# Performance work log

Measured on AMD Instinct MI355X. Metric: run time of the kernel, lower is better.

## Reference

```python
import jax, jax.numpy as jnp
import numpy as np

B, C, U, N = 8, 64, 3, 512


def setup_inputs() -> dict:
    key = jax.random.key(0)
    k1, k2, k3, k4 = jax.random.split(key, 4)
    x = jax.random.normal(k1, (B, C, U, N), dtype=jnp.float32)
    # nn.Linear weights [out, in], applied as x @ W.T over channel dim
    s = 1.0 / np.sqrt(C)
    Wq = jax.random.uniform(k2, (C, C), dtype=jnp.float32, minval=-s, maxval=s)
    Wk = jax.random.uniform(k3, (C, C), dtype=jnp.float32, minval=-s, maxval=s)
    Wv = jax.random.uniform(k4, (C, C), dtype=jnp.float32, minval=-s, maxval=s)
    return {"x": x, "Wq": Wq, "Wk": Wk, "Wv": Wv}


def reference(x, Wq, Wk, Wv):
    # VNLinear: Linear over channel dim (dim 1), no bias: out[b,d,u,n] = sum_c x[b,c,u,n] W[d,c]
    def vn_linear(t, W):
        return jnp.einsum('bcun,dc->bdun', t, W)

    q = vn_linear(x, Wq)
    k = vn_linear(x, Wk)
    v = vn_linear(x, Wv)
    scale = x.shape[1] ** (-0.5)  # in_channels^-0.5
    # contraction over tiny vector-neuron dim u=3
    attn_logits = jnp.einsum('bcui,bcuj->bcij', q, k) * scale  # [B,C,N,N]
    attn_weights = jax.nn.softmax(attn_logits, axis=-1)
    out = jnp.einsum('bcij,bcuj->bcui', attn_weights, v)  # [B,C,U,N]
    return x + out
```

## Files before the change

kernel.cpp:

```cpp
#include <hip/hip_runtime.h>

#define BB 8
#define CC 64
#define UU 3
#define NN 512
#define POS (UU * NN)
#define QKV_ELEMS (BB * CC * POS)
#define SCALE2 0.1803368801111793f

typedef float f2 __attribute__((ext_vector_type(2)));

__global__ __launch_bounds__(256) void proj_kernel(
    const float* __restrict__ x,
    const float* __restrict__ Wq,
    const float* __restrict__ Wk,
    const float* __restrict__ Wv,
    float* __restrict__ ws)
{
    const int blk  = blockIdx.x;
    const int b    = blk & 7;
    const int rest = blk >> 3;
    const int d0   = (rest / 6) * 4;
    const int chunk= rest % 6;
    const int p    = chunk * 256 + threadIdx.x;

    const float* wq = Wq + (size_t)d0 * CC;
    const float* wk = Wk + (size_t)d0 * CC;
    const float* wv = Wv + (size_t)d0 * CC;
    const float* xb = x + (size_t)b * CC * POS + p;

    float qa[4] = {0.f, 0.f, 0.f, 0.f};
    float ka[4] = {0.f, 0.f, 0.f, 0.f};
    float va[4] = {0.f, 0.f, 0.f, 0.f};

    #pragma unroll 4
    for (int c = 0; c < CC; ++c) {
        float xv = xb[c * POS];
        #pragma unroll
        for (int r = 0; r < 4; ++r) {
            qa[r] = fmaf(xv, wq[r * CC + c], qa[r]);
            ka[r] = fmaf(xv, wk[r * CC + c], ka[r]);
            va[r] = fmaf(xv, wv[r * CC + c], va[r]);
        }
    }

    float* qs = ws;
    float* ks = ws + QKV_ELEMS;
    float* vs = ws + 2 * QKV_ELEMS;
    #pragma unroll
    for (int r = 0; r < 4; ++r) {
        size_t base = (size_t)(b * CC + d0 + r) * POS + p;
        qs[base] = qa[r] * SCALE2;
        ks[base] = ka[r];
        vs[base] = va[r];
    }
}

__global__ __launch_bounds__(256) void attn_kernel(
    const float* __restrict__ x,
    const float* __restrict__ ws,
    float* __restrict__ out)
{
    const int bd  = blockIdx.x;
    const int tid = threadIdx.x;

    __shared__ __align__(16) float ks[UU][NN];
    __shared__ __align__(16) float vs[UU][NN];
    __shared__ float4 part[NN];

    const float* qsg = ws + (size_t)bd * POS;
    const float* ksg = ws + QKV_ELEMS     + (size_t)bd * POS;
    const float* vsg = ws + 2 * QKV_ELEMS + (size_t)bd * POS;

    {
        const float4* kg4 = (const float4*)ksg;
        const float4* vg4 = (const float4*)vsg;
        float4* ks4 = (float4*)&ks[0][0];
        float4* vs4 = (float4*)&vs[0][0];
        #pragma unroll
        for (int it = 0; it < 3; ++it) {
            int idx = tid + it * 256;
            if (idx < 384) ks4[idx] = kg4[idx];
            else           vs4[idx - 384] = vg4[idx - 384];
        }
    }
    __syncthreads();

    const int h    = tid & 3;
    const int slot = tid >> 2;

    f2 Q0[8], Q1[8], Q2[8];
    #pragma unroll
    for (int m = 0; m < 8; ++m) {
        int i = slot + m * 64;
        float a = qsg[i], b = qsg[NN + i], c = qsg[2 * NN + i];
        Q0[m] = (f2){a, a};
        Q1[m] = (f2){b, b};
        Q2[m] = (f2){c, c};
    }

    f2 L[8], A0[8], A1[8], A2[8];
    #pragma unroll
    for (int m = 0; m < 8; ++m) {
        L[m] = (f2){0.f, 0.f};  A0[m] = (f2){0.f, 0.f};
        A1[m] = (f2){0.f, 0.f}; A2[m] = (f2){0.f, 0.f};
    }

    const float4* k0p = (const float4*)&ks[0][0] + h * 32;
    const float4* k1p = (const float4*)&ks[1][0] + h * 32;
    const float4* k2p = (const float4*)&ks[2][0] + h * 32;
    const float4* v0p = (const float4*)&vs[0][0] + h * 32;
    const float4* v1p = (const float4*)&vs[1][0] + h * 32;
    const float4* v2p = (const float4*)&vs[2][0] + h * 32;
    const int t0 = 2 * h;

    for (int tt = 0; tt < 32; ++tt) {
        const int t = (tt + t0) & 31;
        float4 k0 = k0p[t];
        float4 k1 = k1p[t];
        float4 k2 = k2p[t];
        float4 v0 = v0p[t];
        float4 v1 = v1p[t];
        float4 v2 = v2p[t];

        f2 k0a = (f2){k0.x, k0.y}, k0b = (f2){k0.z, k0.w};
        f2 k1a = (f2){k1.x, k1.y}, k1b = (f2){k1.z, k1.w};
        f2 k2a = (f2){k2.x, k2.y}, k2b = (f2){k2.z, k2.w};
        f2 v0a = (f2){v0.x, v0.y}, v0b = (f2){v0.z, v0.w};
        f2 v1a = (f2){v1.x, v1.y}, v1b = (f2){v1.z, v1.w};
        f2 v2a = (f2){v2.x, v2.y}, v2b = (f2){v2.z, v2.w};

        #pragma unroll
        for (int m = 0; m < 8; ++m) {
            f2 sa = __builtin_elementwise_fma(Q0[m], k0a,
                     __builtin_elementwise_fma(Q1[m], k1a, Q2[m] * k2a));
            f2 sb = __builtin_elementwise_fma(Q0[m], k0b,
                     __builtin_elementwise_fma(Q1[m], k1b, Q2[m] * k2b));

            f2 pa = (f2){__builtin_amdgcn_exp2f(sa.x), __builtin_amdgcn_exp2f(sa.y)};
            f2 pb = (f2){__builtin_amdgcn_exp2f(sb.x), __builtin_amdgcn_exp2f(sb.y)};

            L[m]  = L[m] + pa + pb;
            A0[m] = __builtin_elementwise_fma(pa, v0a,
                      __builtin_elementwise_fma(pb, v0b, A0[m]));
            A1[m] = __builtin_elementwise_fma(pa, v1a,
                      __builtin_elementwise_fma(pb, v1b, A1[m]));
            A2[m] = __builtin_elementwise_fma(pa, v2a,
                      __builtin_elementwise_fma(pb, v2b, A2[m]));
        }
    }

    #pragma unroll
    for (int m = 0; m < 8; ++m) {
        float l  = L[m].x  + L[m].y;
        float a0 = A0[m].x + A0[m].y;
        float a1 = A1[m].x + A1[m].y;
        float a2 = A2[m].x + A2[m].y;

        l  += __shfl_xor(l,  1);  l  += __shfl_xor(l,  2);
        a0 += __shfl_xor(a0, 1);  a0 += __shfl_xor(a0, 2);
        a1 += __shfl_xor(a1, 1);  a1 += __shfl_xor(a1, 2);
        a2 += __shfl_xor(a2, 1);  a2 += __shfl_xor(a2, 2);

        if (h == 0) part[slot + m * 64] = make_float4(a0, a1, a2, l);
    }
    __syncthreads();

    const float* xd = x   + (size_t)bd * POS;
    float*       od = out + (size_t)bd * POS;
    #pragma unroll
    for (int w = 0; w < 2; ++w) {
        int i = tid + w * 256;
        float4 P = part[i];
        float inv = 1.0f / P.w;
        od[i]          = xd[i]          + P.x * inv;
        od[NN + i]     = xd[NN + i]     + P.y * inv;
        od[2 * NN + i] = xd[2 * NN + i] + P.z * inv;
    }
}

__global__ __launch_bounds__(256) void vn_attn_fused(
    const float* __restrict__ x,
    const float* __restrict__ Wq,
    const float* __restrict__ Wk,
    const float* __restrict__ Wv,
    float* __restrict__ out)
{
    const int bd  = blockIdx.x;
    const int b   = bd / CC;
    const int d   = bd % CC;
    const int tid = threadIdx.x;

    __shared__ float wq[CC], wk[CC], wv[CC];
    __shared__ float qs[UU][NN];
    __shared__ float ks[UU][NN];
    __shared__ float vs[UU][NN];

    if (tid < CC) {
        wq[tid] = Wq[d * CC + tid];
        wk[tid] = Wk[d * CC + tid];
        wv[tid] = Wv[d * CC + tid];
    }
    __syncthreads();

    const float* xb = x + (size_t)b * CC * POS;
    for (int p = tid; p < POS; p += 256) {
        float qa = 0.f, ka = 0.f, va = 0.f;
        #pragma unroll 8
        for (int c = 0; c < CC; ++c) {
            float xv = xb[c * POS + p];
            qa = fmaf(xv, wq[c], qa);
            ka = fmaf(xv, wk[c], ka);
            va = fmaf(xv, wv[c], va);
        }
        int u = p >> 9, n = p & (NN - 1);
        qs[u][n] = qa * SCALE2;
        ks[u][n] = ka;
        vs[u][n] = va;
    }
    __syncthreads();

    for (int i = tid; i < NN; i += 256) {
        float q0 = qs[0][i], q1 = qs[1][i], q2 = qs[2][i];
        float l = 0.f, a0 = 0.f, a1 = 0.f, a2 = 0.f;
        for (int j = 0; j < NN; j += 4) {
            float4 k0 = *(const float4*)&ks[0][j];
            float4 k1 = *(const float4*)&ks[1][j];
            float4 k2 = *(const float4*)&ks[2][j];
            float4 v0 = *(const float4*)&vs[0][j];
            float4 v1 = *(const float4*)&vs[1][j];
            float4 v2 = *(const float4*)&vs[2][j];
            float s0 = fmaf(q0, k0.x, fmaf(q1, k1.x, q2 * k2.x));
            float s1 = fmaf(q0, k0.y, fmaf(q1, k1.y, q2 * k2.y));
            float s2 = fmaf(q0, k0.z, fmaf(q1, k1.z, q2 * k2.z));
            float s3 = fmaf(q0, k0.w, fmaf(q1, k1.w, q2 * k2.w));
            float p0 = __builtin_amdgcn_exp2f(s0);
            float p1 = __builtin_amdgcn_exp2f(s1);
            float p2 = __builtin_amdgcn_exp2f(s2);
            float p3 = __builtin_amdgcn_exp2f(s3);
            l += p0 + p1 + p2 + p3;
            a0 = fmaf(p0, v0.x, fmaf(p1, v0.y, fmaf(p2, v0.z, fmaf(p3, v0.w, a0))));
            a1 = fmaf(p0, v1.x, fmaf(p1, v1.y, fmaf(p2, v1.z, fmaf(p3, v1.w, a1))));
            a2 = fmaf(p0, v2.x, fmaf(p1, v2.y, fmaf(p2, v2.z, fmaf(p3, v2.w, a2))));
        }
        float inv = 1.0f / l;
        size_t obase = ((size_t)(b * CC + d) * UU) * NN + i;
        const float* xd = xb + (size_t)d * POS;
        out[obase]          = xd[i]          + a0 * inv;
        out[obase + NN]     = xd[NN + i]     + a1 * inv;
        out[obase + 2 * NN] = xd[2 * NN + i] + a2 * inv;
    }
}

extern "C" void kernel_launch(void* const* d_in, const int* in_sizes, int n_in,
                              void* d_out, int out_size, void* d_ws, size_t ws_size,
                              hipStream_t stream) {
    const float* x  = (const float*)d_in[0];
    const float* Wq = (const float*)d_in[1];
    const float* Wk = (const float*)d_in[2];
    const float* Wv = (const float*)d_in[3];
    float* out = (float*)d_out;

    if (ws_size >= (size_t)3 * QKV_ELEMS * sizeof(float)) {
        float* ws = (float*)d_ws;
        proj_kernel<<<dim3(8 * 16 * 6), dim3(256), 0, stream>>>(x, Wq, Wk, Wv, ws);
        attn_kernel<<<dim3(BB * CC), dim3(256), 0, stream>>>(x, ws, out);
    } else {
        vn_attn_fused<<<dim3(BB * CC), dim3(256), 0, stream>>>(x, Wq, Wk, Wv, out);
    }
}
```

Baseline: 100.6 us.

## Fuse QKV projection into attention kernel, dropping workspace round-trip and second launch

Each block now computes its own q, k, v rows for one (b,d) pair directly from x into shared memory, using packed 2-wide FMAs, instead of a separate projection kernel writing to global workspace. This removes the extra kernel launch and the global write/read of roughly 9.4 MB of q/k/v. In exchange each block rereads the full 64-channel slab of x for its batch (64 blocks share it, so it is mostly L2-served), and shared memory use grows with the added q buffer.

```diff
diff --git a/kernel.cpp b/kernel.cpp
--- a/kernel.cpp
+++ b/kernel.cpp
@@ -5,84 +5,72 @@
 #define UU 3
 #define NN 512
 #define POS (UU * NN)
-#define QKV_ELEMS (BB * CC * POS)
 #define SCALE2 0.1803368801111793f
 
 typedef float f2 __attribute__((ext_vector_type(2)));
 
-__global__ __launch_bounds__(256) void proj_kernel(
+__global__ __launch_bounds__(256) void vn_fused_kernel(
     const float* __restrict__ x,
     const float* __restrict__ Wq,
     const float* __restrict__ Wk,
     const float* __restrict__ Wv,
-    float* __restrict__ ws)
-{
-    const int blk  = blockIdx.x;
-    const int b    = blk & 7;
-    const int rest = blk >> 3;
-    const int d0   = (rest / 6) * 4;
-    const int chunk= rest % 6;
-    const int p    = chunk * 256 + threadIdx.x;
-
-    const float* wq = Wq + (size_t)d0 * CC;
-    const float* wk = Wk + (size_t)d0 * CC;
-    const float* wv = Wv + (size_t)d0 * CC;
-    const float* xb = x + (size_t)b * CC * POS + p;
-
-    float qa[4] = {0.f, 0.f, 0.f, 0.f};
-    float ka[4] = {0.f, 0.f, 0.f, 0.f};
-    float va[4] = {0.f, 0.f, 0.f, 0.f};
-
-    #pragma unroll 4
-    for (int c = 0; c < CC; ++c) {
-        float xv = xb[c * POS];
-        #pragma unroll
-        for (int r = 0; r < 4; ++r) {
-            qa[r] = fmaf(xv, wq[r * CC + c], qa[r]);
-            ka[r] = fmaf(xv, wk[r * CC + c], ka[r]);
-            va[r] = fmaf(xv, wv[r * CC + c], va[r]);
-        }
-    }
-
-    float* qs = ws;
-    float* ks = ws + QKV_ELEMS;
-    float* vs = ws + 2 * QKV_ELEMS;
-    #pragma unroll
-    for (int r = 0; r < 4; ++r) {
-        size_t base = (size_t)(b * CC + d0 + r) * POS + p;
-        qs[base] = qa[r] * SCALE2;
-        ks[base] = ka[r];
-        vs[base] = va[r];
-    }
-}
-
-__global__ __launch_bounds__(256) void attn_kernel(
-    const float* __restrict__ x,
-    const float* __restrict__ ws,
     float* __restrict__ out)
 {
     const int bd  = blockIdx.x;
+    const int b   = bd >> 6;
+    const int d   = bd & 63;
     const int tid = threadIdx.x;
 
+    __shared__ float w[3][CC];
+    __shared__ __align__(16) float qs[UU][NN];
     __shared__ __align__(16) float ks[UU][NN];
     __shared__ __align__(16) float vs[UU][NN];
     __shared__ float4 part[NN];
 
-    const float* qsg = ws + (size_t)bd * POS;
-    const float* ksg = ws + QKV_ELEMS     + (size_t)bd * POS;
-    const float* vsg = ws + 2 * QKV_ELEMS + (size_t)bd * POS;
+    if (tid < 192) {
+        int r = tid >> 6, c = tid & 63;
+        const float* W = (r == 0) ? Wq : (r == 1) ? Wk : Wv;
+        w[r][c] = W[d * CC + c];
+    }
+    __syncthreads();
 
     {
-        const float4* kg4 = (const float4*)ksg;
-        const float4* vg4 = (const float4*)vsg;
-        float4* ks4 = (float4*)&ks[0][0];
-        float4* vs4 = (float4*)&vs[0][0];
-        #pragma unroll
-        for (int it = 0; it < 3; ++it) {
-            int idx = tid + it * 256;
-            if (idx < 384) ks4[idx] = kg4[idx];
-            else           vs4[idx - 384] = vg4[idx - 384];
+        const float* xb = x + (size_t)b * CC * POS;
+        const int p0 = tid * 2;
+
+        f2 qa0 = {0.f,0.f}, qa1 = {0.f,0.f}, qa2 = {0.f,0.f};
+        f2 ka0 = {0.f,0.f}, ka1 = {0.f,0.f}, ka2 = {0.f,0.f};
+        f2 va0 = {0.f,0.f}, va1 = {0.f,0.f}, va2 = {0.f,0.f};
+
+        #pragma unroll 4
+        for (int c = 0; c < CC; ++c) {
+            const float* xc = xb + c * POS + p0;
+            f2 x0 = *(const f2*)(xc);
+            f2 x1 = *(const f2*)(xc + NN);
+            f2 x2 = *(const f2*)(xc + 2 * NN);
+            float wqc = w[0][c], wkc = w[1][c], wvc = w[2][c];
+            f2 wq2 = {wqc, wqc}, wk2 = {wkc, wkc}, wv2 = {wvc, wvc};
+            qa0 = __builtin_elementwise_fma(x0, wq2, qa0);
+            qa1 = __builtin_elementwise_fma(x1, wq2, qa1);
+            qa2 = __builtin_elementwise_fma(x2, wq2, qa2);
+            ka0 = __builtin_elementwise_fma(x0, wk2, ka0);
+            ka1 = __builtin_elementwise_fma(x1, wk2, ka1);
+            ka2 = __builtin_elementwise_fma(x2, wk2, ka2);
+            va0 = __builtin_elementwise_fma(x0, wv2, va0);
+            va1 = __builtin_elementwise_fma(x1, wv2, va1);
+            va2 = __builtin_elementwise_fma(x2, wv2, va2);
         }
+
+        f2 sc = {SCALE2, SCALE2};
+        *(f2*)&qs[0][p0] = qa0 * sc;
+        *(f2*)&qs[1][p0] = qa1 * sc;
+        *(f2*)&qs[2][p0] = qa2 * sc;
+        *(f2*)&ks[0][p0] = ka0;
+        *(f2*)&ks[1][p0] = ka1;
+        *(f2*)&ks[2][p0] = ka2;
+        *(f2*)&vs[0][p0] = va0;
+        *(f2*)&vs[1][p0] = va1;
+        *(f2*)&vs[2][p0] = va2;
     }
     __syncthreads();
 
@@ -93,9 +81,9 @@
     #pragma unroll
     for (int m = 0; m < 8; ++m) {
         int i = slot + m * 64;
-        float a = qsg[i], b = qsg[NN + i], c = qsg[2 * NN + i];
+        float a = qs[0][i], bq = qs[1][i], c = qs[2][i];
         Q0[m] = (f2){a, a};
-        Q1[m] = (f2){b, b};
+        Q1[m] = (f2){bq, bq};
         Q2[m] = (f2){c, c};
     }
 
@@ -169,86 +157,13 @@
     const float* xd = x   + (size_t)bd * POS;
     float*       od = out + (size_t)bd * POS;
     #pragma unroll
-    for (int w = 0; w < 2; ++w) {
-        int i = tid + w * 256;
+    for (int wi = 0; wi < 2; ++wi) {
+        int i = tid + wi * 256;
         float4 P = part[i];
         float inv = 1.0f / P.w;
         od[i]          = xd[i]          + P.x * inv;
         od[NN + i]     = xd[NN + i]     + P.y * inv;
         od[2 * NN + i] = xd[2 * NN + i] + P.z * inv;
-    }
-}
-
-__global__ __launch_bounds__(256) void vn_attn_fused(
-    const float* __restrict__ x,
-    const float* __restrict__ Wq,
-    const float* __restrict__ Wk,
-    const float* __restrict__ Wv,
-    float* __restrict__ out)
-{
-    const int bd  = blockIdx.x;
-    const int b   = bd / CC;
-    const int d   = bd % CC;
-    const int tid = threadIdx.x;
-
-    __shared__ float wq[CC], wk[CC], wv[CC];
-    __shared__ float qs[UU][NN];
-    __shared__ float ks[UU][NN];
-    __shared__ float vs[UU][NN];
-
-    if (tid < CC) {
-        wq[tid] = Wq[d * CC + tid];
-        wk[tid] = Wk[d * CC + tid];
-        wv[tid] = Wv[d * CC + tid];
-    }
-    __syncthreads();
-
-    const float* xb = x + (size_t)b * CC * POS;
-    for (int p = tid; p < POS; p += 256) {
-        float qa = 0.f, ka = 0.f, va = 0.f;
-        #pragma unroll 8
-        for (int c = 0; c < CC; ++c) {
-            float xv = xb[c * POS + p];
-            qa = fmaf(xv, wq[c], qa);
-            ka = fmaf(xv, wk[c], ka);
-            va = fmaf(xv, wv[c], va);
-        }
-        int u = p >> 9, n = p & (NN - 1);
-        qs[u][n] = qa * SCALE2;
-        ks[u][n] = ka;
-        vs[u][n] = va;
-    }
-    __syncthreads();
-
-    for (int i = tid; i < NN; i += 256) {
-        float q0 = qs[0][i], q1 = qs[1][i], q2 = qs[2][i];
-        float l = 0.f, a0 = 0.f, a1 = 0.f, a2 = 0.f;
-        for (int j = 0; j < NN; j += 4) {
-            float4 k0 = *(const float4*)&ks[0][j];
-            float4 k1 = *(const float4*)&ks[1][j];
-            float4 k2 = *(const float4*)&ks[2][j];
-            float4 v0 = *(const float4*)&vs[0][j];
-            float4 v1 = *(const float4*)&vs[1][j];
-            float4 v2 = *(const float4*)&vs[2][j];
-            float s0 = fmaf(q0, k0.x, fmaf(q1, k1.x, q2 * k2.x));
-            float s1 = fmaf(q0, k0.y, fmaf(q1, k1.y, q2 * k2.y));
-            float s2 = fmaf(q0, k0.z, fmaf(q1, k1.z, q2 * k2.z));
-            float s3 = fmaf(q0, k0.w, fmaf(q1, k1.w, q2 * k2.w));
-            float p0 = __builtin_amdgcn_exp2f(s0);
-            float p1 = __builtin_amdgcn_exp2f(s1);
-            float p2 = __builtin_amdgcn_exp2f(s2);
-            float p3 = __builtin_amdgcn_exp2f(s3);
-            l += p0 + p1 + p2 + p3;
-            a0 = fmaf(p0, v0.x, fmaf(p1, v0.y, fmaf(p2, v0.z, fmaf(p3, v0.w, a0))));
-            a1 = fmaf(p0, v1.x, fmaf(p1, v1.y, fmaf(p2, v1.z, fmaf(p3, v1.w, a1))));
-            a2 = fmaf(p0, v2.x, fmaf(p1, v2.y, fmaf(p2, v2.z, fmaf(p3, v2.w, a2))));
-        }
-        float inv = 1.0f / l;
-        size_t obase = ((size_t)(b * CC + d) * UU) * NN + i;
-        const float* xd = xb + (size_t)d * POS;
-        out[obase]          = xd[i]          + a0 * inv;
-        out[obase + NN]     = xd[NN + i]     + a1 * inv;
-        out[obase + 2 * NN] = xd[2 * NN + i] + a2 * inv;
     }
 }
 
@@ -261,11 +176,5 @@
     const float* Wv = (const float*)d_in[3];
     float* out = (float*)d_out;
 
-    if (ws_size >= (size_t)3 * QKV_ELEMS * sizeof(float)) {
-        float* ws = (float*)d_ws;
-        proj_kernel<<<dim3(8 * 16 * 6), dim3(256), 0, stream>>>(x, Wq, Wk, Wv, ws);
-        attn_kernel<<<dim3(BB * CC), dim3(256), 0, stream>>>(x, ws, out);
-    } else {
-        vn_attn_fused<<<dim3(BB * CC), dim3(256), 0, stream>>>(x, Wq, Wk, Wv, out);
-    }
+    vn_fused_kernel<<<dim3(BB * CC), dim3(256), 0, stream>>>(x, Wq, Wk, Wv, out);
 }
```

After: 97.82 us. -2.8%, faster.
